# Kernel tuning notes

Measured on AMD Instinct MI355X. Metric: run time of the kernel, lower is better.

Reference implementation:

```python
import jax, jax.numpy as jnp
import numpy as np

N_NODES = 100000
N_EDGES = 1600000
N_GRAPHS = 64
IN_F = 128
H_F = 128
N_CLS = 10


def setup_inputs() -> dict:
    key = jax.random.key(0)
    ks = jax.random.split(key, 10)
    feat = jax.random.normal(ks[0], (N_NODES, IN_F), dtype=jnp.float32)
    W1 = jax.random.normal(ks[1], (IN_F, H_F), dtype=jnp.float32) * 0.05
    b1 = jax.random.normal(ks[2], (H_F,), dtype=jnp.float32) * 0.05
    W2 = jax.random.normal(ks[3], (H_F, H_F), dtype=jnp.float32) * 0.05
    b2 = jax.random.normal(ks[4], (H_F,), dtype=jnp.float32) * 0.05
    Wp = jax.random.normal(ks[5], (H_F, N_CLS), dtype=jnp.float32) * 0.05
    bp = jax.random.normal(ks[6], (N_CLS,), dtype=jnp.float32) * 0.05
    src = jax.random.randint(ks[7], (N_EDGES,), 0, N_NODES, dtype=jnp.int32)
    dst = jax.random.randint(ks[8], (N_EDGES,), 0, N_NODES, dtype=jnp.int32)
    graph_id = jnp.sort(jax.random.randint(ks[9], (N_NODES,), 0, N_GRAPHS, dtype=jnp.int32))
    return {"feat": feat, "W1": W1, "b1": b1, "W2": W2, "b2": b2,
            "Wp": Wp, "bp": bp, "src": src, "dst": dst, "graph_id": graph_id}


def reference(feat, W1, b1, W2, b2, Wp, bp, src, dst, graph_id):
    # copy_u + sum: each dst node sums features of its source neighbors
    def agg(h):
        return jax.ops.segment_sum(h[src], dst, num_segments=N_NODES)

    h = jax.nn.relu(agg(feat) @ W1 + b1)   # conv1 + ReLU
    h = jax.nn.relu(agg(h) @ W2 + b2)      # conv2 + ReLU (num_messagepasses=2)

    # dgl.mean_nodes: per-graph mean pooling over nodes
    sums = jax.ops.segment_sum(h, graph_id, num_segments=N_GRAPHS)      # [G, H]
    cnts = jax.ops.segment_sum(jnp.ones((N_NODES, 1), h.dtype), graph_id,
                               num_segments=N_GRAPHS)                    # [G, 1]
    graph_feats = sums / jnp.maximum(cnts, 1.0)
    return graph_feats @ Wp + bp
```

## Files before the change

### kernel.cpp

```cpp
#include <hip/hip_runtime.h>

#define NF 128
#define NGRAPHS 64
#define NCLS 10
#define NPARTS 256
#define PART_SHIFT 9
#define PART_NODES 512
#define PART_CAP 9216
#define SPLIT_TILE 4096
#define AS_STRIDE 136
#define SRC_BITS 17

typedef __attribute__((ext_vector_type(8))) short bf16x8;
typedef __attribute__((ext_vector_type(4))) float f32x4;
typedef __attribute__((ext_vector_type(8))) unsigned short u16x8;

__device__ __forceinline__ float bf2f(unsigned short u) {
    union { unsigned int i; float f; } v; v.i = ((unsigned int)u) << 16; return v.f;
}
__device__ __forceinline__ unsigned short f2bf(float f) {
    union { float f; unsigned int i; } v; v.f = f;
    unsigned int lsb = (v.i >> 16) & 1;
    v.i += 0x7fffu + lsb;
    return (unsigned short)(v.i >> 16);
}

__global__ __launch_bounds__(256) void split_prep_kernel(
    const int* __restrict__ src, const int* __restrict__ dst,
    unsigned int* __restrict__ records, int* __restrict__ gcur,
    const float* __restrict__ feat, unsigned short* __restrict__ featbf,
    const float* __restrict__ W1, const float* __restrict__ W2,
    unsigned short* __restrict__ Wt1, unsigned short* __restrict__ Wt2,
    float* __restrict__ sums, int ne, int nv4) {
    __shared__ unsigned int stage[SPLIT_TILE];
    __shared__ int hcnt[NPARTS];
    __shared__ int hscan[NPARTS];
    __shared__ int hcur[NPARTS];
    __shared__ int hg[NPARTS];
    int t = threadIdx.x;
    int gtid = blockIdx.x * 256 + t;
    int nthreads = gridDim.x * 256;

    for (int i = gtid; i < nv4; i += nthreads) {
        float4 v = ((const float4*)feat)[i];
        ushort4 o;
        o.x = f2bf(v.x); o.y = f2bf(v.y); o.z = f2bf(v.z); o.w = f2bf(v.w);
        ((ushort4*)featbf)[i] = o;
    }
    for (int i = gtid; i < 2 * NF * NF; i += nthreads) {
        const float* W = (i < NF * NF) ? W1 : W2;
        unsigned short* Wt = (i < NF * NF) ? Wt1 : Wt2;
        int id = i & (NF * NF - 1);
        int f = id >> 7;
        int k = id & 127;
        Wt[f * NF + k] = f2bf(W[k * NF + f]);
    }
    for (int i = gtid; i < NGRAPHS * NF; i += nthreads) sums[i] = 0.f;

    int tile0 = blockIdx.x * SPLIT_TILE;
    int cnt = min(SPLIT_TILE, ne - tile0);
    if (cnt <= 0) return;
    hcnt[t] = 0;
    __syncthreads();
    int dv[16], sv[16];
#pragma unroll
    for (int k2 = 0; k2 < 16; ++k2) {
        int i = k2 * 256 + t;
        if (i < cnt) {
            dv[k2] = dst[tile0 + i];
            sv[k2] = src[tile0 + i];
            atomicAdd(&hcnt[dv[k2] >> PART_SHIFT], 1);
        }
    }
    __syncthreads();
    hscan[t] = hcnt[t];
    __syncthreads();
    for (int off = 1; off < NPARTS; off <<= 1) {
        int v = (t >= off) ? hscan[t - off] : 0;
        __syncthreads();
        hscan[t] += v;
        __syncthreads();
    }
    hcur[t] = hscan[t] - hcnt[t];
    hg[t] = hcnt[t] ? atomicAdd(&gcur[t], hcnt[t]) : 0;
    __syncthreads();
#pragma unroll
    for (int k2 = 0; k2 < 16; ++k2) {
        int i = k2 * 256 + t;
        if (i < cnt) {
            int d = dv[k2];
            int pos = atomicAdd(&hcur[d >> PART_SHIFT], 1);
            stage[pos] = (((unsigned int)(d & (PART_NODES - 1))) << SRC_BITS)
                         | (unsigned int)sv[k2];
        }
    }
    __syncthreads();
    int grp = t >> 4;
    int lt = t & 15;
    for (int p = grp; p < NPARTS; p += 16) {
        int c = hcnt[p];
        if (c == 0) continue;
        int b = hscan[p] - c;
        int g = hg[p];
        if (g + c > PART_CAP) c = max(0, PART_CAP - g);
        unsigned int* outp = records + (size_t)p * PART_CAP + g;
        for (int i = lt; i < c; i += 16) outp[i] = stage[b + i];
    }
}

__global__ __launch_bounds__(256) void build_kernel(
    const unsigned int* __restrict__ records, const int* __restrict__ gcur,
    int* __restrict__ offs, int* __restrict__ eid, int n) {
    __shared__ int deg[PART_NODES];
    __shared__ int ps[NPARTS];
    __shared__ int wsum[4];
    __shared__ unsigned int rc[PART_CAP];
    int t = threadIdx.x;
    int p = blockIdx.x;

    ps[t] = min(gcur[t], PART_CAP);
    __syncthreads();
    for (int off = 1; off < NPARTS; off <<= 1) {
        int v = (t >= off) ? ps[t - off] : 0;
        __syncthreads();
        ps[t] += v;
        __syncthreads();
    }
    int L = min(gcur[p], PART_CAP);
    int base_g = ps[p] - L;
    if (p == 0 && t == 0) offs[n] = ps[NPARTS - 1];

    int lo = p << PART_SHIFT;
    int nn = min(n - lo, PART_NODES);
    if (nn <= 0) return;

    deg[t] = 0;
    deg[t + 256] = 0;
    __syncthreads();

    const unsigned int* rp = records + (size_t)p * PART_CAP;
    for (int i = t; i < L; i += 256) {
        unsigned int r = rp[i];
        rc[i] = r;
        atomicAdd(&deg[r >> SRC_BITS], 1);
    }
    __syncthreads();

    int v0 = deg[2 * t];
    int v1 = deg[2 * t + 1];
    int tsum = v0 + v1;
    int lane = t & 63, w = t >> 6;
    int sc = tsum;
    for (int off = 1; off < 64; off <<= 1) {
        int u = __shfl_up(sc, off, 64);
        if (lane >= off) sc += u;
    }
    if (lane == 63) wsum[w] = sc;
    __syncthreads();
    if (t == 0) {
        int a = 0;
        for (int k = 0; k < 4; ++k) { int v = wsum[k]; wsum[k] = a; a += v; }
    }
    __syncthreads();
    int run = sc - tsum + wsum[w];
    deg[2 * t] = run;
    if (2 * t < nn) offs[lo + 2 * t] = base_g + run;
    run += v0;
    deg[2 * t + 1] = run;
    if (2 * t + 1 < nn) offs[lo + 2 * t + 1] = base_g + run;
    __syncthreads();

    for (int i = t; i < L; i += 256) {
        unsigned int r = rc[i];
        int pos = atomicAdd(&deg[r >> SRC_BITS], 1);
        eid[base_g + pos] = (int)(r & ((1u << SRC_BITS) - 1));
    }
}

__global__ __launch_bounds__(256) void gather_gemm1(
    const unsigned short* __restrict__ x, const int* __restrict__ offs,
    const int* __restrict__ eid, const unsigned short* __restrict__ Wt,
    const float* __restrict__ bias, unsigned short* __restrict__ out, int n) {
    __shared__ unsigned short As[16 * AS_STRIDE];
    int wave = threadIdx.x >> 6;
    int lane = threadIdx.x & 63;
    int q = lane >> 4;
    int c = lane & 15;
    int node_base = blockIdx.x * 16;

    for (int i = 0; i < 4; ++i) {
        int row = wave * 4 + i;
        int node = node_base + row;
        float acc[8] = {0.f, 0.f, 0.f, 0.f, 0.f, 0.f, 0.f, 0.f};
        if (node < n) {
            int beg = offs[node];
            int end = offs[node + 1];
            int j = beg + q;
            for (; j + 4 < end; j += 8) {
                int s0 = eid[j];
                int s1 = eid[j + 4];
                u16x8 v0 = ((const u16x8*)(x + (size_t)s0 * NF))[c];
                u16x8 v1 = ((const u16x8*)(x + (size_t)s1 * NF))[c];
#pragma unroll
                for (int r = 0; r < 8; ++r) acc[r] += bf2f(v0[r]) + bf2f(v1[r]);
            }
            if (j < end) {
                int s0 = eid[j];
                u16x8 v0 = ((const u16x8*)(x + (size_t)s0 * NF))[c];
#pragma unroll
                for (int r = 0; r < 8; ++r) acc[r] += bf2f(v0[r]);
            }
        }
#pragma unroll
        for (int r = 0; r < 8; ++r) acc[r] += __shfl_xor(acc[r], 16, 64);
#pragma unroll
        for (int r = 0; r < 8; ++r) acc[r] += __shfl_xor(acc[r], 32, 64);
        if (q == 0) {
            u16x8 o;
#pragma unroll
            for (int r = 0; r < 8; ++r) o[r] = f2bf(acc[r]);
            *(u16x8*)(&As[row * AS_STRIDE + c * 8]) = o;
        }
    }
    __syncthreads();

    int m16 = c;
    int n0 = wave * 32;
    const unsigned short* b0r = Wt + (size_t)(n0 + m16) * NF + q * 8;
    const unsigned short* b1r = b0r + 16 * NF;
    f32x4 acc0 = {0.f, 0.f, 0.f, 0.f};
    f32x4 acc1 = {0.f, 0.f, 0.f, 0.f};
#pragma unroll
    for (int kk = 0; kk < 4; ++kk) {
        bf16x8 a  = *(const bf16x8*)(&As[m16 * AS_STRIDE + kk * 32 + q * 8]);
        bf16x8 b0 = *(const bf16x8*)(b0r + kk * 32);
        bf16x8 b1 = *(const bf16x8*)(b1r + kk * 32);
        acc0 = __builtin_amdgcn_mfma_f32_16x16x32_bf16(a, b0, acc0, 0, 0, 0);
        acc1 = __builtin_amdgcn_mfma_f32_16x16x32_bf16(a, b1, acc1, 0, 0, 0);
    }
    float bias0 = bias[n0 + m16];
    float bias1 = bias[n0 + 16 + m16];
#pragma unroll
    for (int r = 0; r < 4; ++r) {
        int node = node_base + q * 4 + r;
        if (node >= n) break;
        unsigned short* o = out + (size_t)node * NF;
        o[n0 + m16]      = f2bf(fmaxf(acc0[r] + bias0, 0.f));
        o[n0 + 16 + m16] = f2bf(fmaxf(acc1[r] + bias1, 0.f));
    }
}

__global__ __launch_bounds__(256) void gather_gemm2_pool(
    const unsigned short* __restrict__ x, const int* __restrict__ offs,
    const int* __restrict__ eid, const unsigned short* __restrict__ Wt,
    const float* __restrict__ bias, const int* __restrict__ gid,
    float* __restrict__ sums, int n) {
    __shared__ unsigned short As[16 * AS_STRIDE];
    __shared__ float hblk[16][NF];
    int wave = threadIdx.x >> 6;
    int lane = threadIdx.x & 63;
    int q = lane >> 4;
    int c = lane & 15;
    int node_base = blockIdx.x * 16;

    for (int i = 0; i < 4; ++i) {
        int row = wave * 4 + i;
        int node = node_base + row;
        float acc[8] = {0.f, 0.f, 0.f, 0.f, 0.f, 0.f, 0.f, 0.f};
        if (node < n) {
            int beg = offs[node];
            int end = offs[node + 1];
            int j = beg + q;
            for (; j + 4 < end; j += 8) {
                int s0 = eid[j];
                int s1 = eid[j + 4];
                u16x8 v0 = ((const u16x8*)(x + (size_t)s0 * NF))[c];
                u16x8 v1 = ((const u16x8*)(x + (size_t)s1 * NF))[c];
#pragma unroll
                for (int r = 0; r < 8; ++r) acc[r] += bf2f(v0[r]) + bf2f(v1[r]);
            }
            if (j < end) {
                int s0 = eid[j];
                u16x8 v0 = ((const u16x8*)(x + (size_t)s0 * NF))[c];
#pragma unroll
                for (int r = 0; r < 8; ++r) acc[r] += bf2f(v0[r]);
            }
        }
#pragma unroll
        for (int r = 0; r < 8; ++r) acc[r] += __shfl_xor(acc[r], 16, 64);
#pragma unroll
        for (int r = 0; r < 8; ++r) acc[r] += __shfl_xor(acc[r], 32, 64);
        if (q == 0) {
            u16x8 o;
#pragma unroll
            for (int r = 0; r < 8; ++r) o[r] = f2bf(acc[r]);
            *(u16x8*)(&As[row * AS_STRIDE + c * 8]) = o;
        }
    }
    __syncthreads();

    int m16 = c;
    int n0 = wave * 32;
    const unsigned short* b0r = Wt + (size_t)(n0 + m16) * NF + q * 8;
    const unsigned short* b1r = b0r + 16 * NF;
    f32x4 acc0 = {0.f, 0.f, 0.f, 0.f};
    f32x4 acc1 = {0.f, 0.f, 0.f, 0.f};
#pragma unroll
    for (int kk = 0; kk < 4; ++kk) {
        bf16x8 a  = *(const bf16x8*)(&As[m16 * AS_STRIDE + kk * 32 + q * 8]);
        bf16x8 b0 = *(const bf16x8*)(b0r + kk * 32);
        bf16x8 b1 = *(const bf16x8*)(b1r + kk * 32);
        acc0 = __builtin_amdgcn_mfma_f32_16x16x32_bf16(a, b0, acc0, 0, 0, 0);
        acc1 = __builtin_amdgcn_mfma_f32_16x16x32_bf16(a, b1, acc1, 0, 0, 0);
    }
    float bias0 = bias[n0 + m16];
    float bias1 = bias[n0 + 16 + m16];
#pragma unroll
    for (int r = 0; r < 4; ++r) {
        int row = q * 4 + r;
        hblk[row][n0 + m16]      = fmaxf(acc0[r] + bias0, 0.f);
        hblk[row][n0 + 16 + m16] = fmaxf(acc1[r] + bias1, 0.f);
    }
    __syncthreads();

    int t = threadIdx.x;
    if (t < NF) {
        float acc = 0.f;
        int cur = -1;
        int lim = min(16, n - node_base);
        for (int i = 0; i < lim; ++i) {
            int g = gid[node_base + i];
            if (g != cur) {
                if (cur >= 0) atomicAdd(&sums[cur * NF + t], acc);
                acc = 0.f;
                cur = g;
            }
            acc += bf2f(f2bf(hblk[i][t]));
        }
        if (cur >= 0) atomicAdd(&sums[cur * NF + t], acc);
    }
}

__device__ __forceinline__ int lower_bound_i(const int* a, int n, int key) {
    int lo = 0, hi = n;
    while (lo < hi) {
        int mid = (lo + hi) >> 1;
        if (a[mid] < key) lo = mid + 1; else hi = mid;
    }
    return lo;
}

__global__ __launch_bounds__(64) void final_kernel(
    const float* __restrict__ sums, const int* __restrict__ gid, int n,
    const float* __restrict__ Wp, const float* __restrict__ bp,
    float* __restrict__ out) {
    __shared__ int range[2];
    int g = blockIdx.x;
    int c = threadIdx.x;
    if (c == 0) range[0] = lower_bound_i(gid, n, g);
    if (c == 1) range[1] = lower_bound_i(gid, n, g + 1);
    __syncthreads();
    if (c >= NCLS) return;
    float cnt = fmaxf((float)(range[1] - range[0]), 1.0f);
    float inv = 1.0f / cnt;
    float acc = bp[c];
#pragma unroll 8
    for (int k = 0; k < NF; ++k) {
        acc += sums[g * NF + k] * inv * Wp[k * NCLS + c];
    }
    out[g * NCLS + c] = acc;
}

extern "C" void kernel_launch(void* const* d_in, const int* in_sizes, int n_in,
                              void* d_out, int out_size, void* d_ws, size_t ws_size,
                              hipStream_t stream) {
    const float* feat = (const float*)d_in[0];
    const float* W1   = (const float*)d_in[1];
    const float* b1   = (const float*)d_in[2];
    const float* W2   = (const float*)d_in[3];
    const float* b2   = (const float*)d_in[4];
    const float* Wp   = (const float*)d_in[5];
    const float* bp   = (const float*)d_in[6];
    const int*   src  = (const int*)d_in[7];
    const int*   dst  = (const int*)d_in[8];
    const int*   gid  = (const int*)d_in[9];

    int ne = in_sizes[7];
    int n  = in_sizes[9];

    unsigned short* featbf = (unsigned short*)d_ws;
    unsigned short* h1     = featbf + (size_t)n * NF;
    unsigned int* records = (unsigned int*)(h1 + (size_t)n * NF);
    int* eid      = (int*)(records + (size_t)NPARTS * PART_CAP);
    float* sums   = (float*)(eid + ne);
    int* gcur     = (int*)(sums + NGRAPHS * NF);
    unsigned short* Wt1 = (unsigned short*)(gcur + NPARTS);
    unsigned short* Wt2 = Wt1 + NF * NF;
    int* offs     = (int*)(Wt2 + NF * NF);

    int nv4 = n * NF / 4;
    int splitblocks = (ne + SPLIT_TILE - 1) / SPLIT_TILE;
    int buildblocks = (n + PART_NODES - 1) >> PART_SHIFT;
    int ggblocks = (n + 15) / 16;

    hipMemsetAsync(gcur, 0, NPARTS * sizeof(int), stream);
    split_prep_kernel<<<splitblocks, 256, 0, stream>>>(
        src, dst, records, gcur, feat, featbf, W1, W2, Wt1, Wt2, sums, ne, nv4);
    build_kernel<<<buildblocks, 256, 0, stream>>>(records, gcur, offs, eid, n);

    gather_gemm1<<<ggblocks, 256, 0, stream>>>(featbf, offs, eid, Wt1, b1, h1, n);
    gather_gemm2_pool<<<ggblocks, 256, 0, stream>>>(h1, offs, eid, Wt2, b2, gid, sums, n);
    final_kernel<<<NGRAPHS, 64, 0, stream>>>(sums, gid, n, Wp, bp, (float*)d_out);
}
```

Measured before the change: 316.0 us.

## Replace global atomic partition cursors with per-tile count tables and binary-search gather

The split kernel no longer reserves space with global atomics on per-partition cursors and scatters into partition buckets. Each tile now writes its locally sorted records contiguously and stores per-partition counts and offsets. The build kernel scans those tile counts, then uses a binary search to gather each partition's records from all tiles. This drops the memset and the atomic contention, and makes the record writes coalesced. In exchange the gather reads are scattered, CSR offsets are per-partition fixed bases with a separate degree array, and the gather kernels read the degree array to find where each row ends.

```diff
diff --git a/kernel.cpp b/kernel.cpp
--- a/kernel.cpp
+++ b/kernel.cpp
@@ -8,6 +8,7 @@
 #define PART_NODES 512
 #define PART_CAP 9216
 #define SPLIT_TILE 4096
+#define MAX_TILES 512
 #define AS_STRIDE 136
 #define SRC_BITS 17
 
@@ -27,7 +28,8 @@
 
 __global__ __launch_bounds__(256) void split_prep_kernel(
     const int* __restrict__ src, const int* __restrict__ dst,
-    unsigned int* __restrict__ records, int* __restrict__ gcur,
+    unsigned int* __restrict__ records, int* __restrict__ cnts,
+    int* __restrict__ hbase_g,
     const float* __restrict__ feat, unsigned short* __restrict__ featbf,
     const float* __restrict__ W1, const float* __restrict__ W2,
     unsigned short* __restrict__ Wt1, unsigned short* __restrict__ Wt2,
@@ -36,7 +38,6 @@
     __shared__ int hcnt[NPARTS];
     __shared__ int hscan[NPARTS];
     __shared__ int hcur[NPARTS];
-    __shared__ int hg[NPARTS];
     int t = threadIdx.x;
     int gtid = blockIdx.x * 256 + t;
     int nthreads = gridDim.x * 256;
@@ -82,7 +83,8 @@
         __syncthreads();
     }
     hcur[t] = hscan[t] - hcnt[t];
-    hg[t] = hcnt[t] ? atomicAdd(&gcur[t], hcnt[t]) : 0;
+    cnts[(size_t)blockIdx.x * NPARTS + t] = hcnt[t];
+    hbase_g[(size_t)blockIdx.x * NPARTS + t] = hscan[t] - hcnt[t];
     __syncthreads();
 #pragma unroll
     for (int k2 = 0; k2 < 16; ++k2) {
@@ -95,60 +97,33 @@
         }
     }
     __syncthreads();
-    int grp = t >> 4;
-    int lt = t & 15;
-    for (int p = grp; p < NPARTS; p += 16) {
-        int c = hcnt[p];
-        if (c == 0) continue;
-        int b = hscan[p] - c;
-        int g = hg[p];
-        if (g + c > PART_CAP) c = max(0, PART_CAP - g);
-        unsigned int* outp = records + (size_t)p * PART_CAP + g;
-        for (int i = lt; i < c; i += 16) outp[i] = stage[b + i];
-    }
+    for (int i = t; i < cnt; i += 256) records[tile0 + i] = stage[i];
 }
 
 __global__ __launch_bounds__(256) void build_kernel(
-    const unsigned int* __restrict__ records, const int* __restrict__ gcur,
-    int* __restrict__ offs, int* __restrict__ eid, int n) {
+    const unsigned int* __restrict__ records, const int* __restrict__ cnts,
+    const int* __restrict__ hbase_g, int* __restrict__ offs,
+    int* __restrict__ degs, int* __restrict__ eid, int n, int ntiles) {
     __shared__ int deg[PART_NODES];
-    __shared__ int ps[NPARTS];
+    __shared__ int pref[MAX_TILES + 1];
+    __shared__ int hb[MAX_TILES];
+    __shared__ unsigned int rc[PART_CAP];
     __shared__ int wsum[4];
-    __shared__ unsigned int rc[PART_CAP];
+    __shared__ int Ltot;
     int t = threadIdx.x;
     int p = blockIdx.x;
-
-    ps[t] = min(gcur[t], PART_CAP);
-    __syncthreads();
-    for (int off = 1; off < NPARTS; off <<= 1) {
-        int v = (t >= off) ? ps[t - off] : 0;
-        __syncthreads();
-        ps[t] += v;
-        __syncthreads();
-    }
-    int L = min(gcur[p], PART_CAP);
-    int base_g = ps[p] - L;
-    if (p == 0 && t == 0) offs[n] = ps[NPARTS - 1];
-
     int lo = p << PART_SHIFT;
     int nn = min(n - lo, PART_NODES);
     if (nn <= 0) return;
 
     deg[t] = 0;
     deg[t + 256] = 0;
-    __syncthreads();
-
-    const unsigned int* rp = records + (size_t)p * PART_CAP;
-    for (int i = t; i < L; i += 256) {
-        unsigned int r = rp[i];
-        rc[i] = r;
-        atomicAdd(&deg[r >> SRC_BITS], 1);
-    }
-    __syncthreads();
-
-    int v0 = deg[2 * t];
-    int v1 = deg[2 * t + 1];
-    int tsum = v0 + v1;
+
+    int i0 = 2 * t, i1 = 2 * t + 1;
+    int c0 = 0, c1 = 0;
+    if (i0 < ntiles) { c0 = cnts[(size_t)i0 * NPARTS + p]; hb[i0] = hbase_g[(size_t)i0 * NPARTS + p]; }
+    if (i1 < ntiles) { c1 = cnts[(size_t)i1 * NPARTS + p]; hb[i1] = hbase_g[(size_t)i1 * NPARTS + p]; }
+    int tsum = c0 + c1;
     int lane = t & 63, w = t >> 6;
     int sc = tsum;
     for (int off = 1; off < 64; off <<= 1) {
@@ -160,14 +135,52 @@
     if (t == 0) {
         int a = 0;
         for (int k = 0; k < 4; ++k) { int v = wsum[k]; wsum[k] = a; a += v; }
+        Ltot = a;
     }
     __syncthreads();
     int run = sc - tsum + wsum[w];
-    deg[2 * t] = run;
-    if (2 * t < nn) offs[lo + 2 * t] = base_g + run;
-    run += v0;
-    deg[2 * t + 1] = run;
-    if (2 * t + 1 < nn) offs[lo + 2 * t + 1] = base_g + run;
+    if (i0 < ntiles) pref[i0] = run;
+    run += c0;
+    if (i1 < ntiles) pref[i1] = run;
+    if (t == 0) pref[ntiles] = Ltot;
+    __syncthreads();
+
+    int L = min(Ltot, PART_CAP);
+
+    for (int i = t; i < L; i += 256) {
+        int lo2 = 0, hi2 = ntiles;
+        while (lo2 + 1 < hi2) {
+            int mid = (lo2 + hi2) >> 1;
+            if (pref[mid] <= i) lo2 = mid; else hi2 = mid;
+        }
+        unsigned int r = records[(size_t)lo2 * SPLIT_TILE + hb[lo2] + (i - pref[lo2])];
+        rc[i] = r;
+        atomicAdd(&deg[r >> SRC_BITS], 1);
+    }
+    __syncthreads();
+
+    int v0 = deg[2 * t];
+    int v1 = deg[2 * t + 1];
+    int tsum2 = v0 + v1;
+    int sc2 = tsum2;
+    for (int off = 1; off < 64; off <<= 1) {
+        int u = __shfl_up(sc2, off, 64);
+        if (lane >= off) sc2 += u;
+    }
+    if (lane == 63) wsum[w] = sc2;
+    __syncthreads();
+    if (t == 0) {
+        int a = 0;
+        for (int k = 0; k < 4; ++k) { int v = wsum[k]; wsum[k] = a; a += v; }
+    }
+    __syncthreads();
+    int run2 = sc2 - tsum2 + wsum[w];
+    int base_g = p * PART_CAP;
+    deg[2 * t] = run2;
+    if (2 * t < nn) { offs[lo + 2 * t] = base_g + run2; degs[lo + 2 * t] = v0; }
+    run2 += v0;
+    deg[2 * t + 1] = run2;
+    if (2 * t + 1 < nn) { offs[lo + 2 * t + 1] = base_g + run2; degs[lo + 2 * t + 1] = v1; }
     __syncthreads();
 
     for (int i = t; i < L; i += 256) {
@@ -179,7 +192,8 @@
 
 __global__ __launch_bounds__(256) void gather_gemm1(
     const unsigned short* __restrict__ x, const int* __restrict__ offs,
-    const int* __restrict__ eid, const unsigned short* __restrict__ Wt,
+    const int* __restrict__ degs, const int* __restrict__ eid,
+    const unsigned short* __restrict__ Wt,
     const float* __restrict__ bias, unsigned short* __restrict__ out, int n) {
     __shared__ unsigned short As[16 * AS_STRIDE];
     int wave = threadIdx.x >> 6;
@@ -194,7 +208,7 @@
         float acc[8] = {0.f, 0.f, 0.f, 0.f, 0.f, 0.f, 0.f, 0.f};
         if (node < n) {
             int beg = offs[node];
-            int end = offs[node + 1];
+            int end = beg + degs[node];
             int j = beg + q;
             for (; j + 4 < end; j += 8) {
                 int s0 = eid[j];
@@ -252,7 +266,8 @@
 
 __global__ __launch_bounds__(256) void gather_gemm2_pool(
     const unsigned short* __restrict__ x, const int* __restrict__ offs,
-    const int* __restrict__ eid, const unsigned short* __restrict__ Wt,
+    const int* __restrict__ degs, const int* __restrict__ eid,
+    const unsigned short* __restrict__ Wt,
     const float* __restrict__ bias, const int* __restrict__ gid,
     float* __restrict__ sums, int n) {
     __shared__ unsigned short As[16 * AS_STRIDE];
@@ -269,7 +284,7 @@
         float acc[8] = {0.f, 0.f, 0.f, 0.f, 0.f, 0.f, 0.f, 0.f};
         if (node < n) {
             int beg = offs[node];
-            int end = offs[node + 1];
+            int end = beg + degs[node];
             int j = beg + q;
             for (; j + 4 < end; j += 8) {
                 int s0 = eid[j];
@@ -388,27 +403,31 @@
     int ne = in_sizes[7];
     int n  = in_sizes[9];
 
+    int ntiles = (ne + SPLIT_TILE - 1) / SPLIT_TILE;
+
     unsigned short* featbf = (unsigned short*)d_ws;
     unsigned short* h1     = featbf + (size_t)n * NF;
     unsigned int* records = (unsigned int*)(h1 + (size_t)n * NF);
-    int* eid      = (int*)(records + (size_t)NPARTS * PART_CAP);
-    float* sums   = (float*)(eid + ne);
-    int* gcur     = (int*)(sums + NGRAPHS * NF);
-    unsigned short* Wt1 = (unsigned short*)(gcur + NPARTS);
+    int* eid      = (int*)(records + ne);
+    float* sums   = (float*)(eid + (size_t)NPARTS * PART_CAP);
+    int* cnts     = (int*)(sums + NGRAPHS * NF);
+    int* hbase_g  = cnts + (size_t)ntiles * NPARTS;
+    unsigned short* Wt1 = (unsigned short*)(hbase_g + (size_t)ntiles * NPARTS);
     unsigned short* Wt2 = Wt1 + NF * NF;
     int* offs     = (int*)(Wt2 + NF * NF);
+    int* degs     = offs + n;
 
     int nv4 = n * NF / 4;
-    int splitblocks = (ne + SPLIT_TILE - 1) / SPLIT_TILE;
     int buildblocks = (n + PART_NODES - 1) >> PART_SHIFT;
     int ggblocks = (n + 15) / 16;
 
-    hipMemsetAsync(gcur, 0, NPARTS * sizeof(int), stream);
-    split_prep_kernel<<<splitblocks, 256, 0, stream>>>(
-        src, dst, records, gcur, feat, featbf, W1, W2, Wt1, Wt2, sums, ne, nv4);
-    build_kernel<<<buildblocks, 256, 0, stream>>>(records, gcur, offs, eid, n);
-
-    gather_gemm1<<<ggblocks, 256, 0, stream>>>(featbf, offs, eid, Wt1, b1, h1, n);
-    gather_gemm2_pool<<<ggblocks, 256, 0, stream>>>(h1, offs, eid, Wt2, b2, gid, sums, n);
+    split_prep_kernel<<<ntiles, 256, 0, stream>>>(
+        src, dst, records, cnts, hbase_g, feat, featbf, W1, W2, Wt1, Wt2,
+        sums, ne, nv4);
+    build_kernel<<<buildblocks, 256, 0, stream>>>(
+        records, cnts, hbase_g, offs, degs, eid, n, ntiles);
+
+    gather_gemm1<<<ggblocks, 256, 0, stream>>>(featbf, offs, degs, eid, Wt1, b1, h1, n);
+    gather_gemm2_pool<<<ggblocks, 256, 0, stream>>>(h1, offs, degs, eid, Wt2, b2, gid, sums, n);
     final_kernel<<<NGRAPHS, 64, 0, stream>>>(sums, gid, n, Wp, bp, (float*)d_out);
 }
```

After: 330.5 us. 1.05x slower.
